# Optimization experiments

Measured on AMD Instinct MI355X. Metric: run time of the kernel, lower is better.

Reference implementation:

```python
import jax, jax.numpy as jnp
import numpy as np
import math

N_HEAD = 8
N_FEAT = 512
D_K = N_FEAT // N_HEAD
B, T = 4, 2048


def setup_inputs() -> dict:
    key = jax.random.key(0)
    ks = jax.random.split(key, 16)
    s = 1.0 / math.sqrt(N_FEAT)
    return {
        "x": jax.random.normal(ks[0], (B, T, N_FEAT), dtype=jnp.float32),
        "pos_emb": jax.random.normal(ks[1], (1, T, N_FEAT), dtype=jnp.float32),
        "Wq": jax.random.normal(ks[2], (N_FEAT, N_FEAT), dtype=jnp.float32) * s,
        "bq": jnp.zeros((N_FEAT,), dtype=jnp.float32),
        "Wk": jax.random.normal(ks[3], (N_FEAT, N_FEAT), dtype=jnp.float32) * s,
        "bk": jnp.zeros((N_FEAT,), dtype=jnp.float32),
        "Wv": jax.random.normal(ks[4], (N_FEAT, N_FEAT), dtype=jnp.float32) * s,
        "bv": jnp.zeros((N_FEAT,), dtype=jnp.float32),
        "Wpos": jax.random.normal(ks[5], (N_FEAT, N_FEAT), dtype=jnp.float32) * s,
        "Wout": jax.random.normal(ks[6], (N_FEAT, N_FEAT), dtype=jnp.float32) * s,
        "bout": jnp.zeros((N_FEAT,), dtype=jnp.float32),
        "pos_bias_u": jax.random.normal(ks[7], (N_HEAD, D_K), dtype=jnp.float32) * 0.05,
        "pos_bias_v": jax.random.normal(ks[8], (N_HEAD, D_K), dtype=jnp.float32) * 0.05,
    }


def reference(x, pos_emb, Wq, bq, Wk, bk, Wv, bv, Wpos, Wout, bout,
              pos_bias_u, pos_bias_v):
    b, t, f = x.shape
    h, d = N_HEAD, D_K
    # QKV projections (torch Linear: y = x @ W.T + b), split into heads -> (B,H,T,d)
    q = (jnp.einsum('btf,of->bto', x, Wq) + bq).reshape(b, t, h, d).transpose(0, 2, 1, 3)
    k = (jnp.einsum('btf,of->bto', x, Wk) + bk).reshape(b, t, h, d).transpose(0, 2, 1, 3)
    v = (jnp.einsum('btf,of->bto', x, Wv) + bv).reshape(b, t, h, d).transpose(0, 2, 1, 3)
    # positional projection: (1, T_pos, F) -> (H, T_pos, d)
    tp = pos_emb.shape[1]
    p = jnp.einsum('ptf,of->pto', pos_emb, Wpos).reshape(tp, h, d).transpose(1, 0, 2)
    q_u = q + pos_bias_u[None, :, None, :]  # (B,H,T,d)
    q_v = q + pos_bias_v[None, :, None, :]
    matrix_ac = jnp.einsum('bhtd,bhsd->bhts', q_u, k)   # content-content
    matrix_bd = jnp.einsum('bhtd,hsd->bhts', q_v, p)    # content-position
    scores = (matrix_ac + matrix_bd) / math.sqrt(d)
    attn = jax.nn.softmax(scores, axis=-1)  # dropout is identity in eval mode
    out = jnp.einsum('bhts,bhsd->bhtd', attn, v)
    out = out.transpose(0, 2, 1, 3).reshape(b, t, h * d)
    return jnp.einsum('btf,of->bto', out, Wout) + bout
```

## Files before the change

### kernel.cpp

```cpp
#include <hip/hip_runtime.h>

typedef float f4 __attribute__((ext_vector_type(4)));
typedef __attribute__((ext_vector_type(8))) short bf16x8;
typedef __attribute__((ext_vector_type(4))) float f32x4;
typedef __attribute__((ext_vector_type(2))) int i32x2;

#define T_SEQ 2048
#define NFEAT 512
#define NHEAD 8
#define DK    64
#define BATCH 4

using gptr_t = const __attribute__((address_space(1))) void*;
using lptr_t = __attribute__((address_space(3))) void*;

#define LOG2E_8 0.18033688011f

static __device__ __forceinline__ short f2bf(float f) {
    unsigned u = __builtin_bit_cast(unsigned, f);
    u += 0x7fff + ((u >> 16) & 1);
    return (short)(u >> 16);
}
static __device__ __forceinline__ float b2f(short s) {
    unsigned u = ((unsigned)(unsigned short)s) << 16;
    return __builtin_bit_cast(float, u);
}
static __device__ __forceinline__ int pkbf(float a, float b) {
    unsigned ua = __builtin_bit_cast(unsigned, a) + 0x8000u;
    unsigned ub = __builtin_bit_cast(unsigned, b) + 0x8000u;
    return (int)((ua >> 16) | (ub & 0xFFFF0000u));
}

__global__ __launch_bounds__(256) void cvt_kernel(
    const float* __restrict__ x, const float* __restrict__ pos,
    const float* __restrict__ Wq, const float* __restrict__ Wk, const float* __restrict__ Wv,
    const float* __restrict__ Wpos, const float* __restrict__ Wout,
    const float* __restrict__ bq, const float* __restrict__ bk, const float* __restrict__ bv,
    short* __restrict__ xb, short* __restrict__ posb, short* __restrict__ wqkv,
    short* __restrict__ wpb, short* __restrict__ wob, float* __restrict__ bqkv)
{
    const int blk = blockIdx.x;
    const float* src; short* dst; int off;
    if      (blk < 2048) { src = x;    dst = xb;          off = blk * 2048; }
    else if (blk < 2560) { src = pos;  dst = posb;        off = (blk - 2048) * 2048; }
    else if (blk < 2688) { src = Wq;   dst = wqkv;        off = (blk - 2560) * 2048; }
    else if (blk < 2816) { src = Wk;   dst = wqkv + 262144; off = (blk - 2688) * 2048; }
    else if (blk < 2944) { src = Wv;   dst = wqkv + 524288; off = (blk - 2816) * 2048; }
    else if (blk < 3072) { src = Wpos; dst = wpb;         off = (blk - 2944) * 2048; }
    else if (blk < 3200) { src = Wout; dst = wob;         off = (blk - 3072) * 2048; }
    else {
        int t = threadIdx.x;
        bqkv[t]        = bq[t];        bqkv[256 + t]  = bq[256 + t];
        bqkv[512 + t]  = bk[t];        bqkv[768 + t]  = bk[256 + t];
        bqkv[1024 + t] = bv[t];        bqkv[1280 + t] = bv[256 + t];
        return;
    }
    int i = off + threadIdx.x * 8;
    f4 a = *(const f4*)(src + i);
    f4 b = *(const f4*)(src + i + 4);
    bf16x8 o;
#pragma unroll
    for (int j = 0; j < 4; ++j) { o[j] = f2bf(a[j]); o[4 + j] = f2bf(b[j]); }
    *(bf16x8*)(dst + i) = o;
}

template<int OUT_BF16>
static __device__ __forceinline__ void gemm_tile(
    short* As, short* Bs,
    const short* __restrict__ A, const short* __restrict__ B,
    const float* __restrict__ bias, void* __restrict__ Cv,
    int N, int K, int row0, int col0)
{
    const int tid = threadIdx.x, lane = tid & 63, wave = tid >> 6;
    const int col = lane & 15, quad = lane >> 4;
    const int wm = (wave >> 1) * 64, wn = (wave & 1) * 64;
    const int rl = lane & 15;

    const short* Abase = A + (size_t)(row0 + wave * 32 + rl) * K + (lane >> 4) * 8;
    const short* Bbase = B + (size_t)(col0 + wave * 32 + rl) * K + (lane >> 4) * 8;

    f32x4 acc[4][4];
#pragma unroll
    for (int i = 0; i < 4; ++i)
#pragma unroll
        for (int j = 0; j < 4; ++j) acc[i][j] = (f32x4){0.f, 0.f, 0.f, 0.f};

    for (int k0 = 0; k0 < K; k0 += 64) {
        __syncthreads();
#pragma unroll
        for (int c = 0; c < 2; ++c)
#pragma unroll
            for (int hf = 0; hf < 2; ++hf) {
                __builtin_amdgcn_global_load_lds((gptr_t)(Abase + (size_t)(16 * c) * K + k0 + hf * 32),
                                                 (lptr_t)(As + wave * 2048 + c * 1024 + hf * 512), 16, 0, 0);
                __builtin_amdgcn_global_load_lds((gptr_t)(Bbase + (size_t)(16 * c) * K + k0 + hf * 32),
                                                 (lptr_t)(Bs + wave * 2048 + c * 1024 + hf * 512), 16, 0, 0);
            }
        __syncthreads();
#pragma unroll
        for (int kt = 0; kt < 2; ++kt) {
            bf16x8 af[4], bfr[4];
#pragma unroll
            for (int mt = 0; mt < 4; ++mt)
                af[mt] = *(const bf16x8*)&As[((wm >> 4) + mt) * 1024 + (kt * 4 + quad) * 128 + col * 8];
#pragma unroll
            for (int nt = 0; nt < 4; ++nt)
                bfr[nt] = *(const bf16x8*)&Bs[((wn >> 4) + nt) * 1024 + (kt * 4 + quad) * 128 + col * 8];
#pragma unroll
            for (int mt = 0; mt < 4; ++mt)
#pragma unroll
                for (int nt = 0; nt < 4; ++nt)
                    acc[mt][nt] = __builtin_amdgcn_mfma_f32_16x16x32_bf16(af[mt], bfr[nt], acc[mt][nt], 0, 0, 0);
        }
    }

    float bv4[4];
#pragma unroll
    for (int nt = 0; nt < 4; ++nt)
        bv4[nt] = bias ? bias[col0 + wn + nt * 16 + col] : 0.f;
#pragma unroll
    for (int mt = 0; mt < 4; ++mt)
#pragma unroll
        for (int reg = 0; reg < 4; ++reg) {
            int r = row0 + wm + mt * 16 + quad * 4 + reg;
#pragma unroll
            for (int nt = 0; nt < 4; ++nt) {
                int c = col0 + wn + nt * 16 + col;
                float v = acc[mt][nt][reg] + bv4[nt];
                if (OUT_BF16) ((short*)Cv)[(size_t)r * N + c] = f2bf(v);
                else          ((float*)Cv)[(size_t)r * N + c] = v;
            }
        }
}

__global__ __launch_bounds__(256) void gemm_qkv_pos(
    const short* __restrict__ xb, const short* __restrict__ wqkv,
    const float* __restrict__ bqkv, short* __restrict__ QKV,
    const short* __restrict__ posb, const short* __restrict__ wpb,
    short* __restrict__ Pm)
{
    __shared__ short As[8192], Bs[8192];
    const int bid = blockIdx.x;
    if (bid < 768) {
        const int xcd = bid & 7, s = bid >> 3;
        const int row = xcd * 8 + (s & 7), colt = s >> 3;
        gemm_tile<1>(As, Bs, xb, wqkv, bqkv, QKV, 1536, 512, row * 128, colt * 128);
    } else {
        const int t = bid - 768;
        gemm_tile<1>(As, Bs, posb, wpb, nullptr, Pm, 512, 512, (t / 4) * 128, (t % 4) * 128);
    }
}

__global__ __launch_bounds__(256) void gemm_out_kernel(
    const short* __restrict__ A, const short* __restrict__ B,
    const float* __restrict__ bias, float* __restrict__ C)
{
    __shared__ short As[8192], Bs[8192];
    const int bid = blockIdx.x;
    const int xcd = bid & 7, s = bid >> 3;
    const int row = xcd * 8 + (s & 7), colt = s >> 3;
    gemm_tile<0>(As, Bs, A, B, bias, C, 512, 512, row * 128, colt * 128);
}

__global__ __launch_bounds__(256) void kvprep_kernel(
    const short* __restrict__ qkv, const short* __restrict__ pm,
    const float* __restrict__ u, const float* __restrict__ vb,
    short* __restrict__ kp, short* __restrict__ vt, float* __restrict__ cb)
{
    __shared__ short tile[64][72];
    const int tid = threadIdx.x, lr = tid >> 2, lc = (tid & 3) * 16;
    const int bh = blockIdx.y, b = bh >> 3, h = bh & 7, s0 = blockIdx.x * 64;

    const short* kptr = qkv + (size_t)(b * T_SEQ + s0 + lr) * 1536 + 512 + h * DK + lc;
    const short* pptr = pm + (size_t)(s0 + lr) * NFEAT + h * DK + lc;
    const short* vptr = qkv + (size_t)(b * T_SEQ + s0 + lr) * 1536 + 1024 + h * DK + lc;
    bf16x8 k0_ = *(const bf16x8*)kptr,       k1_ = *(const bf16x8*)(kptr + 8);
    bf16x8 p0_ = *(const bf16x8*)pptr,       p1_ = *(const bf16x8*)(pptr + 8);
    bf16x8 v0_ = *(const bf16x8*)vptr,       v1_ = *(const bf16x8*)(vptr + 8);

    float c = 0.f;
    bf16x8 o0, o1;
#pragma unroll
    for (int j = 0; j < 8; ++j) {
        float kf = b2f(k0_[j]), pf = b2f(p0_[j]);
        o0[j] = f2bf(kf + pf);
        c += u[h * DK + lc + j] * kf + vb[h * DK + lc + j] * pf;
        float kf1 = b2f(k1_[j]), pf1 = b2f(p1_[j]);
        o1[j] = f2bf(kf1 + pf1);
        c += u[h * DK + lc + 8 + j] * kf1 + vb[h * DK + lc + 8 + j] * pf1;
    }
    short* kpd = kp + ((size_t)bh * T_SEQ + s0 + lr) * DK + lc;
    *(bf16x8*)kpd       = o0;
    *(bf16x8*)(kpd + 8) = o1;
    c += __shfl_xor(c, 1);
    c += __shfl_xor(c, 2);
    if ((tid & 3) == 0) cb[(size_t)bh * T_SEQ + s0 + lr] = LOG2E_8 * c;

    *(bf16x8*)&tile[lr][lc]     = v0_;
    *(bf16x8*)&tile[lr][lc + 8] = v1_;
    __syncthreads();
    short* dst = vt + (size_t)(bh * DK + lr) * T_SEQ + s0 + lc;
    bf16x8 t0_, t1_;
#pragma unroll
    for (int j = 0; j < 8; ++j) { t0_[j] = tile[lc + j][lr]; t1_[j] = tile[lc + 8 + j][lr]; }
    *(bf16x8*)dst       = t0_;
    *(bf16x8*)(dst + 8) = t1_;
}

__global__ __launch_bounds__(256, 4) void attn_kernel(
    const short* __restrict__ qkv, const short* __restrict__ kp,
    const short* __restrict__ vt, const float* __restrict__ cb,
    short* __restrict__ attO)
{
    __shared__ __align__(16) short KPs[64][72], Vts[64][72], Ps[4][32][72];
    __shared__ float cs[64];
    const int tid = threadIdx.x, lane = tid & 63, wave = tid >> 6;
    const int col = lane & 15, quad = lane >> 4;
    const int idx = blockIdx.x;
    const int xcd = idx & 7, slot = idx >> 3;
    const int bh = (slot >> 4) * 8 + xcd;
    const int t0 = (slot & 15) * 128;
    const int b = bh >> 3, h = bh & 7;

    bf16x8 qa[2][2];
#pragma unroll
    for (int g = 0; g < 2; ++g) {
        const short* qb = qkv + (size_t)(b * T_SEQ + t0 + wave * 32 + g * 16 + col) * 1536 + h * DK + quad * 8;
        qa[g][0] = *(const bf16x8*)qb;
        qa[g][1] = *(const bf16x8*)(qb + 32);
    }

    const int lr  = tid >> 2;
    const int lcq = (tid & 3) * 16;
    const int rho = 4 * (lr & 15) + (lr >> 4);

    const short* kpbase = kp + (size_t)bh * T_SEQ * DK;
    const short* vtbase = vt + (size_t)bh * DK * T_SEQ;

    bf16x8 kpr0 = *(const bf16x8*)(kpbase + (size_t)rho * DK + lcq);
    bf16x8 kpr1 = *(const bf16x8*)(kpbase + (size_t)rho * DK + lcq + 8);
    bf16x8 vtr0 = *(const bf16x8*)(vtbase + (size_t)lr * T_SEQ + lcq);
    bf16x8 vtr1 = *(const bf16x8*)(vtbase + (size_t)lr * T_SEQ + lcq + 8);
    float cbr = (tid < 64) ? cb[(size_t)bh * T_SEQ + tid] : 0.f;

    f32x4 Oacc[2][4];
    float lsum[2][4];
#pragma unroll
    for (int g = 0; g < 2; ++g)
#pragma unroll
        for (int i = 0; i < 4; ++i) { Oacc[g][i] = (f32x4){0.f, 0.f, 0.f, 0.f}; lsum[g][i] = 0.f; }

    for (int s0 = 0; s0 < T_SEQ; s0 += 64) {
        __syncthreads();
        *(bf16x8*)&KPs[lr][lcq]     = kpr0;
        *(bf16x8*)&KPs[lr][lcq + 8] = kpr1;
        *(bf16x8*)&Vts[lr][lcq]     = vtr0;
        *(bf16x8*)&Vts[lr][lcq + 8] = vtr1;
        if (tid < 64) cs[tid] = cbr;
        __syncthreads();

        const int sn = (s0 + 64) & (T_SEQ - 1);
        kpr0 = *(const bf16x8*)(kpbase + (size_t)(sn + rho) * DK + lcq);
        kpr1 = *(const bf16x8*)(kpbase + (size_t)(sn + rho) * DK + lcq + 8);
        vtr0 = *(const bf16x8*)(vtbase + (size_t)lr * T_SEQ + sn + lcq);
        vtr1 = *(const bf16x8*)(vtbase + (size_t)lr * T_SEQ + sn + lcq + 8);
        if (tid < 64) cbr = cb[(size_t)bh * T_SEQ + sn + tid];

        f32x4 S[2][4];
#pragma unroll
        for (int g = 0; g < 2; ++g)
#pragma unroll
            for (int nt = 0; nt < 4; ++nt) S[g][nt] = (f32x4){0.f, 0.f, 0.f, 0.f};
#pragma unroll
        for (int nt = 0; nt < 4; ++nt) {
            bf16x8 b0 = *(const bf16x8*)&KPs[nt * 16 + col][quad * 8];
            bf16x8 b1 = *(const bf16x8*)&KPs[nt * 16 + col][32 + quad * 8];
            S[0][nt] = __builtin_amdgcn_mfma_f32_16x16x32_bf16(qa[0][0], b0, S[0][nt], 0, 0, 0);
            S[1][nt] = __builtin_amdgcn_mfma_f32_16x16x32_bf16(qa[1][0], b0, S[1][nt], 0, 0, 0);
            S[0][nt] = __builtin_amdgcn_mfma_f32_16x16x32_bf16(qa[0][1], b1, S[0][nt], 0, 0, 0);
            S[1][nt] = __builtin_amdgcn_mfma_f32_16x16x32_bf16(qa[1][1], b1, S[1][nt], 0, 0, 0);
        }
        const f4 cv = *(const f4*)&cs[4 * col];
#pragma unroll
        for (int g = 0; g < 2; ++g)
#pragma unroll
            for (int reg = 0; reg < 4; ++reg) {
                float e0 = __builtin_amdgcn_exp2f(fmaf(S[0 + g * 0][0][reg], LOG2E_8, cv[0]));
                e0 = __builtin_amdgcn_exp2f(fmaf(S[g][0][reg], LOG2E_8, cv[0]));
                float e1 = __builtin_amdgcn_exp2f(fmaf(S[g][1][reg], LOG2E_8, cv[1]));
                float e2 = __builtin_amdgcn_exp2f(fmaf(S[g][2][reg], LOG2E_8, cv[2]));
                float e3 = __builtin_amdgcn_exp2f(fmaf(S[g][3][reg], LOG2E_8, cv[3]));
                lsum[g][reg] += (e0 + e1) + (e2 + e3);
                i32x2 pw; pw[0] = pkbf(e0, e1); pw[1] = pkbf(e2, e3);
                *(i32x2*)&Ps[wave][g * 16 + quad * 4 + reg][4 * col] = pw;
            }
#pragma unroll
        for (int kt = 0; kt < 2; ++kt) {
            bf16x8 pa0 = *(const bf16x8*)&Ps[wave][col][kt * 32 + quad * 8];
            bf16x8 pa1 = *(const bf16x8*)&Ps[wave][16 + col][kt * 32 + quad * 8];
#pragma unroll
            for (int dt = 0; dt < 4; ++dt) {
                bf16x8 vb = *(const bf16x8*)&Vts[dt * 16 + col][kt * 32 + quad * 8];
                Oacc[0][dt] = __builtin_amdgcn_mfma_f32_16x16x32_bf16(pa0, vb, Oacc[0][dt], 0, 0, 0);
                Oacc[1][dt] = __builtin_amdgcn_mfma_f32_16x16x32_bf16(pa1, vb, Oacc[1][dt], 0, 0, 0);
            }
        }
    }
#pragma unroll
    for (int g = 0; g < 2; ++g)
#pragma unroll
        for (int reg = 0; reg < 4; ++reg) {
            float l = lsum[g][reg];
#pragma unroll
            for (int off = 1; off < 16; off <<= 1) l += __shfl_xor(l, off);
            float inv = 1.f / l;
            int t = t0 + wave * 32 + g * 16 + quad * 4 + reg;
            short* op = attO + (size_t)(b * T_SEQ + t) * NFEAT + h * DK;
#pragma unroll
            for (int dt = 0; dt < 4; ++dt)
                op[dt * 16 + col] = f2bf(Oacc[g][dt][reg] * inv);
        }
}

extern "C" void kernel_launch(void* const* d_in, const int* in_sizes, int n_in,
                              void* d_out, int out_size, void* d_ws, size_t ws_size,
                              hipStream_t stream)
{
    const float* x    = (const float*)d_in[0];
    const float* pos  = (const float*)d_in[1];
    const float* Wq   = (const float*)d_in[2];
    const float* bq   = (const float*)d_in[3];
    const float* Wk   = (const float*)d_in[4];
    const float* bk   = (const float*)d_in[5];
    const float* Wv   = (const float*)d_in[6];
    const float* bv   = (const float*)d_in[7];
    const float* Wpos = (const float*)d_in[8];
    const float* Wout = (const float*)d_in[9];
    const float* bout = (const float*)d_in[10];
    const float* pbu  = (const float*)d_in[11];
    const float* pbv  = (const float*)d_in[12];
    float* out = (float*)d_out;

    short* xb   = (short*)d_ws;
    short* posb = xb   + 4194304;
    short* wqkv = posb + 1048576;
    short* wpb  = wqkv + 786432;
    short* wob  = wpb  + 262144;
    short* QKV  = wob  + 262144;
    short* Pm   = QKV  + 12582912;
    short* KP   = Pm   + 1048576;
    short* Vt   = KP   + 4194304;
    short* AttO = Vt   + 4194304;
    float* bqkv = (float*)(AttO + 4194304);
    float* Cb   = bqkv + 1536;

    cvt_kernel<<<dim3(3201), dim3(256), 0, stream>>>(x, pos, Wq, Wk, Wv, Wpos, Wout, bq, bk, bv,
                                                     xb, posb, wqkv, wpb, wob, bqkv);
    gemm_qkv_pos<<<dim3(832), dim3(256), 0, stream>>>(xb, wqkv, bqkv, QKV, posb, wpb, Pm);
    kvprep_kernel<<<dim3(T_SEQ / 64, BATCH * NHEAD), dim3(256), 0, stream>>>(QKV, Pm, pbu, pbv, KP, Vt, Cb);
    attn_kernel<<<dim3(512), dim3(256), 0, stream>>>(QKV, KP, Vt, Cb, AttO);
    gemm_out_kernel<<<dim3(256), dim3(256), 0, stream>>>(AttO, wob, bout, out);
}
```

Measured before the change: 226.9 us.

## Split attention key range in two halves and add a combine kernel

The attention kernel now splits the key sequence into two halves, launching twice as many blocks. Each block writes unnormalized partial outputs and row sums to a workspace, and a new combine kernel adds the halves and normalizes. This raises parallelism from 512 blocks to fill more CUs, in exchange for an extra kernel launch, extra workspace traffic and bf16 rounding of the partial outputs. The split is safe without max-subtraction because the softmax carries no running max.

```diff
diff --git a/kernel.cpp b/kernel.cpp
--- a/kernel.cpp
+++ b/kernel.cpp
@@ -210,7 +210,7 @@
 __global__ __launch_bounds__(256, 4) void attn_kernel(
     const short* __restrict__ qkv, const short* __restrict__ kp,
     const short* __restrict__ vt, const float* __restrict__ cb,
-    short* __restrict__ attO)
+    short* __restrict__ Op, float* __restrict__ Lb)
 {
     __shared__ __align__(16) short KPs[64][72], Vts[64][72], Ps[4][32][72];
     __shared__ float cs[64];
@@ -218,8 +218,10 @@
     const int col = lane & 15, quad = lane >> 4;
     const int idx = blockIdx.x;
     const int xcd = idx & 7, slot = idx >> 3;
-    const int bh = (slot >> 4) * 8 + xcd;
-    const int t0 = (slot & 15) * 128;
+    const int half = slot & 1;
+    const int t0 = ((slot >> 1) & 15) * 128;
+    const int bh = (slot >> 5) * 8 + xcd;
+    const int base = half * 1024;
     const int b = bh >> 3, h = bh & 7;
 
     bf16x8 qa[2][2];
@@ -237,11 +239,11 @@
     const short* kpbase = kp + (size_t)bh * T_SEQ * DK;
     const short* vtbase = vt + (size_t)bh * DK * T_SEQ;
 
-    bf16x8 kpr0 = *(const bf16x8*)(kpbase + (size_t)rho * DK + lcq);
-    bf16x8 kpr1 = *(const bf16x8*)(kpbase + (size_t)rho * DK + lcq + 8);
-    bf16x8 vtr0 = *(const bf16x8*)(vtbase + (size_t)lr * T_SEQ + lcq);
-    bf16x8 vtr1 = *(const bf16x8*)(vtbase + (size_t)lr * T_SEQ + lcq + 8);
-    float cbr = (tid < 64) ? cb[(size_t)bh * T_SEQ + tid] : 0.f;
+    bf16x8 kpr0 = *(const bf16x8*)(kpbase + (size_t)(base + rho) * DK + lcq);
+    bf16x8 kpr1 = *(const bf16x8*)(kpbase + (size_t)(base + rho) * DK + lcq + 8);
+    bf16x8 vtr0 = *(const bf16x8*)(vtbase + (size_t)lr * T_SEQ + base + lcq);
+    bf16x8 vtr1 = *(const bf16x8*)(vtbase + (size_t)lr * T_SEQ + base + lcq + 8);
+    float cbr = (tid < 64) ? cb[(size_t)bh * T_SEQ + base + tid] : 0.f;
 
     f32x4 Oacc[2][4];
     float lsum[2][4];
@@ -250,7 +252,7 @@
 #pragma unroll
         for (int i = 0; i < 4; ++i) { Oacc[g][i] = (f32x4){0.f, 0.f, 0.f, 0.f}; lsum[g][i] = 0.f; }
 
-    for (int s0 = 0; s0 < T_SEQ; s0 += 64) {
+    for (int it = 0; it < 16; ++it) {
         __syncthreads();
         *(bf16x8*)&KPs[lr][lcq]     = kpr0;
         *(bf16x8*)&KPs[lr][lcq + 8] = kpr1;
@@ -259,7 +261,7 @@
         if (tid < 64) cs[tid] = cbr;
         __syncthreads();
 
-        const int sn = (s0 + 64) & (T_SEQ - 1);
+        const int sn = base + (((it + 1) & 15) << 6);
         kpr0 = *(const bf16x8*)(kpbase + (size_t)(sn + rho) * DK + lcq);
         kpr1 = *(const bf16x8*)(kpbase + (size_t)(sn + rho) * DK + lcq + 8);
         vtr0 = *(const bf16x8*)(vtbase + (size_t)lr * T_SEQ + sn + lcq);
@@ -285,8 +287,7 @@
         for (int g = 0; g < 2; ++g)
 #pragma unroll
             for (int reg = 0; reg < 4; ++reg) {
-                float e0 = __builtin_amdgcn_exp2f(fmaf(S[0 + g * 0][0][reg], LOG2E_8, cv[0]));
-                e0 = __builtin_amdgcn_exp2f(fmaf(S[g][0][reg], LOG2E_8, cv[0]));
+                float e0 = __builtin_amdgcn_exp2f(fmaf(S[g][0][reg], LOG2E_8, cv[0]));
                 float e1 = __builtin_amdgcn_exp2f(fmaf(S[g][1][reg], LOG2E_8, cv[1]));
                 float e2 = __builtin_amdgcn_exp2f(fmaf(S[g][2][reg], LOG2E_8, cv[2]));
                 float e3 = __builtin_amdgcn_exp2f(fmaf(S[g][3][reg], LOG2E_8, cv[3]));
@@ -306,6 +307,8 @@
             }
         }
     }
+    short* ophalf = Op + (size_t)half * 4194304;
+    float* lhalf  = Lb + (size_t)half * 65536 + (size_t)bh * T_SEQ;
 #pragma unroll
     for (int g = 0; g < 2; ++g)
 #pragma unroll
@@ -313,13 +316,32 @@
             float l = lsum[g][reg];
 #pragma unroll
             for (int off = 1; off < 16; off <<= 1) l += __shfl_xor(l, off);
-            float inv = 1.f / l;
             int t = t0 + wave * 32 + g * 16 + quad * 4 + reg;
-            short* op = attO + (size_t)(b * T_SEQ + t) * NFEAT + h * DK;
+            if (col == 0) lhalf[t] = l;
+            short* op = ophalf + (size_t)(b * T_SEQ + t) * NFEAT + h * DK;
 #pragma unroll
             for (int dt = 0; dt < 4; ++dt)
-                op[dt * 16 + col] = f2bf(Oacc[g][dt][reg] * inv);
-        }
+                op[dt * 16 + col] = f2bf(Oacc[g][dt][reg]);
+        }
+}
+
+__global__ __launch_bounds__(256) void combine_kernel(
+    const short* __restrict__ Op, const float* __restrict__ Lb,
+    short* __restrict__ attO)
+{
+    const int e = blockIdx.x * 256 + threadIdx.x;
+    const int flat = e * 8;
+    const int r = flat >> 9, c = flat & 511;
+    const int bh = ((r >> 11) << 3) + (c >> 6);
+    const int t = r & 2047;
+    const float l = Lb[bh * T_SEQ + t] + Lb[65536 + bh * T_SEQ + t];
+    const float inv = 1.f / l;
+    bf16x8 o1 = *(const bf16x8*)(Op + flat);
+    bf16x8 o2 = *(const bf16x8*)(Op + 4194304 + flat);
+    bf16x8 o;
+#pragma unroll
+    for (int j = 0; j < 8; ++j) o[j] = f2bf((b2f(o1[j]) + b2f(o2[j])) * inv);
+    *(bf16x8*)(attO + flat) = o;
 }
 
 extern "C" void kernel_launch(void* const* d_in, const int* in_sizes, int n_in,
@@ -353,11 +375,14 @@
     short* AttO = Vt   + 4194304;
     float* bqkv = (float*)(AttO + 4194304);
     float* Cb   = bqkv + 1536;
+    short* Op   = (short*)(Cb + 65536);
+    float* Lb   = (float*)(Op + 8388608);
 
     cvt_kernel<<<dim3(3201), dim3(256), 0, stream>>>(x, pos, Wq, Wk, Wv, Wpos, Wout, bq, bk, bv,
                                                      xb, posb, wqkv, wpb, wob, bqkv);
     gemm_qkv_pos<<<dim3(832), dim3(256), 0, stream>>>(xb, wqkv, bqkv, QKV, posb, wpb, Pm);
     kvprep_kernel<<<dim3(T_SEQ / 64, BATCH * NHEAD), dim3(256), 0, stream>>>(QKV, Pm, pbu, pbv, KP, Vt, Cb);
-    attn_kernel<<<dim3(512), dim3(256), 0, stream>>>(QKV, KP, Vt, Cb, AttO);
+    attn_kernel<<<dim3(1024), dim3(256), 0, stream>>>(QKV, KP, Vt, Cb, Op, Lb);
+    combine_kernel<<<dim3(2048), dim3(256), 0, stream>>>(Op, Lb, AttO);
     gemm_out_kernel<<<dim3(256), dim3(256), 0, stream>>>(AttO, wob, bout, out);
 }
```

After: 214.0 us. 1.06x faster.
